# Performance work log

Hardware: AMD Instinct MI355X
Metric: run time of the kernel (lower is better)

Reference implementation:

```python
import jax, jax.numpy as jnp
import numpy as np

K_UPPER = 196608  # number of smallest-|grad| positions to mask per sample


def setup_inputs() -> dict:
    key = jax.random.key(0)
    k1, k2 = jax.random.split(key)
    x = jax.random.normal(k1, (64, 3, 512, 512), dtype=jnp.float32)
    grad = jax.random.normal(k2, (64, 3, 512, 512), dtype=jnp.float32)
    return {"x": x, "grad": grad}


def _mask_low_gradient(x, grad):
    # x, grad: [B, C, H, W]
    B, C, H, W = x.shape
    hw = H * W
    flat_g = grad.reshape(B, -1)                                  # [B, C*H*W]
    # _sort: k smallest absolute gradients -> top_k of negated abs (unsorted ok)
    _neg_vals, idx = jax.lax.top_k(-jnp.abs(flat_g), K_UPPER)     # idx: [B, K]
    # channel containing each selected flat index (matches the torch range test)
    ch = idx // hw                                                # [B, K]
    xc = x.reshape(B, C, hw)
    # Faithful to source: torch slice [start:channel_indexes] EXCLUDES the last
    # element of each channel when computing min/max.
    mn = jnp.min(xc[:, :, : hw - 1], axis=-1)                     # [B, C]
    mx = jnp.max(xc[:, :, : hw - 1], axis=-1)                     # [B, C]
    lo = jnp.take_along_axis(mn, ch, axis=1)                      # [B, K]
    hi = jnp.take_along_axis(mx, ch, axis=1)                      # [B, K]
    # uniform fill in [lo, hi) per masked element
    u = jax.random.uniform(jax.random.key(42), idx.shape, dtype=x.dtype)
    fill = lo + u * (hi - lo)                                     # [B, K]
    flat_x = x.reshape(B, -1)
    out = flat_x.at[jnp.arange(B)[:, None], idx].set(fill)
    return out.reshape(x.shape)


def reference(x, grad):
    return _mask_low_gradient(x, grad)
```

## Files before the change

### kernel.cpp

```cpp
#include <hip/hip_runtime.h>
#include <stdint.h>

#define TPB 256
#define TPS 1024

constexpr int BN   = 64;
constexpr int CCH  = 3;
constexpr int HWS  = 262144;
constexpr int LOG_HW = 18;
constexpr int NPS  = 786432;
constexpr int KSEL = 196608;
constexpr int KCAP = 200704;
constexpr int NB_T = 32;
constexpr int CH_T = NPS / NB_T;
constexpr int NB_S = 4;
constexpr int CH_S = KCAP / NB_S;
constexpr int TILE = 4096;
constexpr int NBINS = 2048;
constexpr int SUB  = 8;

constexpr int WS_MN   = 0;
constexpr int WS_MX   = 192;
constexpr int WS_V1   = 384;
constexpr int WS_B1   = 448;
constexpr int WS_GS   = 640;
constexpr int WS_KP   = 704;
constexpr int WS_CNT  = 768;
constexpr int WS_COFF = 2816;
constexpr int WS_MNP  = 4864;
constexpr int WS_MXP  = 6400;
constexpr int WS_THA  = 8192;
constexpr int WS_THB  = WS_THA + BN * NBINS;
constexpr int WS_H0   = WS_THB + BN * NBINS;
constexpr int WS_H1   = WS_H0 + BN * 256 * NB_S;
constexpr int WS_H2   = WS_H1 + BN * 256 * NB_S;
constexpr int WS_H3   = WS_H2 + BN * 256 * NB_S;
constexpr size_t WS_FIX_END = (size_t)WS_H3 + (size_t)BN * 256 * NB_S;
constexpr size_t RECW = (size_t)BN * KCAP * 2;
constexpr size_t WS_NEEDED_BYTES = (WS_FIX_END + 2 * RECW) * 4;

__device__ __forceinline__ unsigned rotl32(unsigned x, int r) { return (x << r) | (x >> (32 - r)); }

__device__ __forceinline__ void tf4(unsigned& x0, unsigned& x1, int a, int b, int c, int d) {
  x0 += x1; x1 = rotl32(x1, a); x1 ^= x0;
  x0 += x1; x1 = rotl32(x1, b); x1 ^= x0;
  x0 += x1; x1 = rotl32(x1, c); x1 ^= x0;
  x0 += x1; x1 = rotl32(x1, d); x1 ^= x0;
}

__device__ __forceinline__ void threefry2x32(unsigned k0, unsigned k1, unsigned c0, unsigned c1,
                                             unsigned& o0, unsigned& o1) {
  const unsigned ks2 = k0 ^ k1 ^ 0x1BD11BDAu;
  unsigned x0 = c0 + k0, x1 = c1 + k1;
  tf4(x0, x1, 13, 15, 26, 6);  x0 += k1;  x1 += ks2 + 1u;
  tf4(x0, x1, 17, 29, 16, 24); x0 += ks2; x1 += k0 + 2u;
  tf4(x0, x1, 13, 15, 26, 6);  x0 += k0;  x1 += k1 + 3u;
  tf4(x0, x1, 17, 29, 16, 24); x0 += k1;  x1 += ks2 + 4u;
  tf4(x0, x1, 13, 15, 26, 6);  x0 += ks2; x1 += k0 + 5u;
  o0 = x0; o1 = x1;
}

__global__ __launch_bounds__(TPB) void k_zero(unsigned* __restrict__ p, int n) {
  int i = blockIdx.x * TPB + threadIdx.x;
  if (i < n) p[i] = 0u;
}

__global__ __launch_bounds__(TPB) void k_copymn(const float4* __restrict__ x,
                                                float4* __restrict__ o,
                                                unsigned* __restrict__ ws) {
  __shared__ float smn[TPB], smx[TPB];
  const int g = blockIdx.x;
  const int bc = g / SUB, sub = g - bc * SUB;
  const int Q4 = HWS / 4 / SUB;
  const size_t base4 = (size_t)bc * (HWS / 4) + (size_t)sub * Q4;
  const bool last = (sub == SUB - 1);
  const int tid = threadIdx.x;
  float lo = 3.4e38f, hi = -3.4e38f;
  for (int i = tid; i < Q4; i += TPB) {
    float4 v = x[base4 + i];
    o[base4 + i] = v;
    if (last && i == Q4 - 1) {
      lo = fminf(lo, fminf(fminf(v.x, v.y), v.z));
      hi = fmaxf(hi, fmaxf(fmaxf(v.x, v.y), v.z));
    } else {
      lo = fminf(lo, fminf(fminf(v.x, v.y), fminf(v.z, v.w)));
      hi = fmaxf(hi, fmaxf(fmaxf(v.x, v.y), fmaxf(v.z, v.w)));
    }
  }
  smn[tid] = lo; smx[tid] = hi; __syncthreads();
  for (int s = TPB / 2; s > 0; s >>= 1) {
    if (tid < s) { smn[tid] = fminf(smn[tid], smn[tid + s]); smx[tid] = fmaxf(smx[tid], smx[tid + s]); }
    __syncthreads();
  }
  if (tid == 0) {
    ((float*)(ws + WS_MNP))[g] = smn[0];
    ((float*)(ws + WS_MXP))[g] = smx[0];
  }
}

__global__ __launch_bounds__(TPB) void k_mnfin(unsigned* __restrict__ ws) {
  const int t = threadIdx.x;
  if (t < BN * CCH) {
    const float* mnp = (const float*)(ws + WS_MNP);
    const float* mxp = (const float*)(ws + WS_MXP);
    float lo = 3.4e38f, hi = -3.4e38f;
    for (int s = 0; s < SUB; ++s) {
      lo = fminf(lo, mnp[t * SUB + s]);
      hi = fmaxf(hi, mxp[t * SUB + s]);
    }
    ((float*)(ws + WS_MN))[t] = lo;
    ((float*)(ws + WS_MX))[t] = hi;
  }
}

__global__ __launch_bounds__(TPB) void k_thrA(const unsigned* __restrict__ gb, unsigned* __restrict__ hist) {
  __shared__ unsigned h[NBINS];
  const int b = blockIdx.y, blk = blockIdx.x, tid = threadIdx.x;
  for (int v = tid; v < NBINS; v += TPB) h[v] = 0u;
  __syncthreads();
  const uint4* g4 = (const uint4*)(gb + (size_t)b * NPS + (size_t)blk * CH_T);
  for (int i = tid; i < CH_T / 4; i += TPB) {
    uint4 v = g4[i];
    atomicAdd(&h[(v.x & 0x7FFFFFFFu) >> 21], 1u);
    atomicAdd(&h[(v.y & 0x7FFFFFFFu) >> 21], 1u);
    atomicAdd(&h[(v.z & 0x7FFFFFFFu) >> 21], 1u);
    atomicAdd(&h[(v.w & 0x7FFFFFFFu) >> 21], 1u);
  }
  __syncthreads();
  unsigned* gh = hist + (size_t)b * NBINS;
  for (int v = tid; v < NBINS; v += TPB) if (h[v]) atomicAdd(&gh[v], h[v]);
}

__global__ __launch_bounds__(TPB) void k_thrB(const unsigned* __restrict__ gb,
                                              unsigned* __restrict__ hist,
                                              const unsigned* __restrict__ ws) {
  __shared__ unsigned h[NBINS];
  const int b = blockIdx.y, blk = blockIdx.x, tid = threadIdx.x;
  for (int v = tid; v < NBINS; v += TPB) h[v] = 0u;
  __syncthreads();
  const unsigned sel = ws[WS_V1 + b];
  const uint4* g4 = (const uint4*)(gb + (size_t)b * NPS + (size_t)blk * CH_T);
  for (int i = tid; i < CH_T / 4; i += TPB) {
    uint4 v = g4[i];
    unsigned a0 = v.x & 0x7FFFFFFFu, a1 = v.y & 0x7FFFFFFFu;
    unsigned a2 = v.z & 0x7FFFFFFFu, a3 = v.w & 0x7FFFFFFFu;
    if ((a0 >> 21) == sel) atomicAdd(&h[(a0 >> 10) & 2047u], 1u);
    if ((a1 >> 21) == sel) atomicAdd(&h[(a1 >> 10) & 2047u], 1u);
    if ((a2 >> 21) == sel) atomicAdd(&h[(a2 >> 10) & 2047u], 1u);
    if ((a3 >> 21) == sel) atomicAdd(&h[(a3 >> 10) & 2047u], 1u);
  }
  __syncthreads();
  unsigned* gh = hist + (size_t)b * NBINS;
  for (int v = tid; v < NBINS; v += TPB) if (h[v]) atomicAdd(&gh[v], h[v]);
}

__global__ __launch_bounds__(TPB) void k_find(const unsigned* __restrict__ hist,
                                              unsigned* __restrict__ ws, int mode) {
  __shared__ unsigned part[TPB];
  const int b = blockIdx.x, tid = threadIdx.x;
  const unsigned* h = hist + (size_t)b * NBINS;
  const int per = NBINS / TPB;
  const unsigned Kt = (mode == 0) ? (unsigned)KSEL : (unsigned)KSEL - ws[WS_B1 + b];
  unsigned vals[8];
  unsigned s = 0;
  for (int j = 0; j < per; ++j) { vals[j] = h[tid * per + j]; s += vals[j]; }
  part[tid] = s; __syncthreads();
  for (int off = 1; off < TPB; off <<= 1) {
    unsigned t = (tid >= off) ? part[tid - off] : 0u;
    __syncthreads(); part[tid] += t; __syncthreads();
  }
  unsigned run = part[tid] - s;
  for (int j = 0; j < per; ++j) {
    const unsigned lo = run, c = vals[j];
    run += c;
    if (lo < Kt && Kt <= run) {
      const unsigned v = (unsigned)(tid * per + j);
      if (mode == 0) {
        ws[WS_V1 + b] = v; ws[WS_B1 + b] = lo;
      } else {
        const unsigned T22 = (ws[WS_V1 + b] << 11) | v;
        ws[WS_GS + b] = (T22 << 10) | 1023u;
        unsigned kp = ws[WS_B1 + b] + lo + c;
        if (kp > (unsigned)KCAP) kp = (unsigned)KCAP;
        ws[WS_KP + b] = kp;
      }
    }
  }
}

__global__ __launch_bounds__(TPB) void k_ccount(const unsigned* __restrict__ gb, unsigned* __restrict__ ws) {
  __shared__ unsigned r[TPB];
  const int b = blockIdx.y, blk = blockIdx.x, tid = threadIdx.x;
  const unsigned G = ws[WS_GS + b];
  const uint4* g4 = (const uint4*)(gb + (size_t)b * NPS + (size_t)blk * CH_T);
  unsigned c = 0;
  for (int i = tid; i < CH_T / 4; i += TPB) {
    uint4 v = g4[i];
    c += (unsigned)((v.x & 0x7FFFFFFFu) <= G) + (unsigned)((v.y & 0x7FFFFFFFu) <= G)
       + (unsigned)((v.z & 0x7FFFFFFFu) <= G) + (unsigned)((v.w & 0x7FFFFFFFu) <= G);
  }
  r[tid] = c; __syncthreads();
  for (int s = TPB / 2; s > 0; s >>= 1) { if (tid < s) r[tid] += r[tid + s]; __syncthreads(); }
  if (tid == 0) ws[WS_CNT + b * NB_T + blk] = r[0];
}

__global__ void k_cscan(unsigned* __restrict__ ws) {
  const int b = blockIdx.x;
  if (threadIdx.x == 0) {
    unsigned run = 0;
    for (int j = 0; j < NB_T; ++j) {
      unsigned t = ws[WS_CNT + b * NB_T + j];
      ws[WS_COFF + b * NB_T + j] = run;
      run += t;
    }
  }
}

__global__ __launch_bounds__(TPB) void k_cscatter(const unsigned* __restrict__ gb,
                                                  const unsigned* __restrict__ ws,
                                                  uint2* __restrict__ outR,
                                                  unsigned* __restrict__ H0) {
  __shared__ unsigned h2[256 * NB_S];
  __shared__ unsigned waveTot[4];
  __shared__ unsigned runBase;
  const int b = blockIdx.y, blk = blockIdx.x, tid = threadIdx.x;
  const int lane = tid & 63, wv = tid >> 6;
  const unsigned long long ltm = (1ull << lane) - 1ull;
  const unsigned G = ws[WS_GS + b];
  for (int e = tid; e < 256 * NB_S; e += TPB) h2[e] = 0u;
  if (tid == 0) runBase = ws[WS_COFF + b * NB_T + blk];
  __syncthreads();
  const unsigned* g = gb + (size_t)b * NPS;
  uint2* oR = outR + (size_t)b * KCAP;
  const unsigned c0 = (unsigned)blk * CH_T;
  for (int t = 0; t < CH_T / 1024; ++t) {
    const unsigned base = c0 + (unsigned)t * 1024u + (unsigned)wv * 256u;
    unsigned key[4], wloc[4];
    bool sel[4];
    unsigned run = 0;
#pragma unroll
    for (int c = 0; c < 4; ++c) {
      const unsigned i = base + (unsigned)c * 64u + (unsigned)lane;
      key[c] = g[i] & 0x7FFFFFFFu;
      sel[c] = (key[c] <= G);
      unsigned long long m = __ballot(sel[c]);
      wloc[c] = run + (unsigned)__popcll(m & ltm);
      run += (unsigned)__popcll(m);
    }
    if (lane == 0) waveTot[wv] = run;
    __syncthreads();
    unsigned wpre = 0;
    for (int w = 0; w < wv; ++w) wpre += waveTot[w];
    const unsigned rb = runBase;
#pragma unroll
    for (int c = 0; c < 4; ++c) {
      if (sel[c]) {
        const unsigned pos = rb + wpre + wloc[c];
        if (pos < (unsigned)KCAP) {
          const unsigned i = base + (unsigned)c * 64u + (unsigned)lane;
          uint2 r; r.x = i; r.y = key[c];
          oR[pos] = r;
          atomicAdd(&h2[(key[c] & 255u) * NB_S + pos / (unsigned)CH_S], 1u);
        }
      }
    }
    __syncthreads();
    if (tid == 0) runBase += waveTot[0] + waveTot[1] + waveTot[2] + waveTot[3];
  }
  __syncthreads();
  unsigned* Hb = H0 + (size_t)b * 256 * NB_S;
  for (int e = tid; e < 256 * NB_S; e += TPB) {
    unsigned c = h2[e];
    if (c) atomicAdd(&Hb[e], c);
  }
}

__global__ __launch_bounds__(TPB) void k_hscan(unsigned* __restrict__ H) {
  __shared__ unsigned wsum[4];
  const int b = blockIdx.x, tid = threadIdx.x;
  const int lane = tid & 63, wv = tid >> 6;
  unsigned* Hb = H + (size_t)b * 256 * NB_S;
  unsigned row[NB_S];
  unsigned run = 0;
#pragma unroll
  for (int k = 0; k < NB_S; ++k) {
    unsigned t = Hb[tid * NB_S + k];
    row[k] = run; run += t;
  }
  unsigned incl = run;
  for (int off = 1; off < 64; off <<= 1) {
    unsigned t = __shfl_up(incl, off, 64);
    if (lane >= off) incl += t;
  }
  if (lane == 63) wsum[wv] = incl;
  __syncthreads();
  unsigned wpre = 0;
  for (int w = 0; w < wv; ++w) wpre += wsum[w];
  const unsigned excl = incl - run + wpre;
#pragma unroll
  for (int k = 0; k < NB_S; ++k) Hb[tid * NB_S + k] = row[k] + excl;
}

template<int FINAL>
__global__ __launch_bounds__(TPS) void k_sort8(const uint2* __restrict__ inR,
                                               uint2* __restrict__ outR,
                                               const unsigned* __restrict__ Hcur,
                                               unsigned* __restrict__ Hnext,
                                               const unsigned* __restrict__ ws,
                                               float* __restrict__ outF,
                                               int shift) {
  __shared__ unsigned wh[16][256];
  __shared__ unsigned gout[256];
  __shared__ unsigned gbase[256];
  __shared__ unsigned wsum[4];
  __shared__ uint2    stg[FINAL ? 1 : TILE];
  __shared__ unsigned h2[FINAL ? 1 : 256 * NB_S];
  const int b = blockIdx.y, blk = blockIdx.x, tid = threadIdx.x;
  const int lane = tid & 63, wv = tid >> 6;
  const unsigned long long ltm = (1ull << lane) - 1ull;
  const unsigned kp = min(ws[WS_KP + b], (unsigned)KCAP);
  const unsigned s0 = (unsigned)blk * CH_S;
  const unsigned s1 = min(s0 + (unsigned)CH_S, kp);
  const uint2* in = inR + (size_t)b * KCAP;
  uint2* out = outR + (size_t)b * KCAP;

  for (int d = tid; d < 256; d += TPS) gbase[d] = Hcur[((size_t)b * 256 + d) * NB_S + blk];
  if (!FINAL) for (int e = tid; e < 256 * NB_S; e += TPS) h2[e] = 0u;
  __syncthreads();

  for (unsigned t0 = s0; t0 < s1; t0 += (unsigned)TILE) {
    { uint4* w4 = (uint4*)&wh[0][0];
      w4[tid] = make_uint4(0u, 0u, 0u, 0u); }
    __syncthreads();

    unsigned key[4], idx[4], wloc[4], dig[4];
    bool val[4];
    const unsigned wbase = t0 + (unsigned)wv * 256u;
#pragma unroll
    for (int c = 0; c < 4; ++c) {
      const unsigned i = wbase + (unsigned)c * 64u + (unsigned)lane;
      val[c] = (i < s1);
      uint2 r = val[c] ? in[i] : make_uint2(0u, 0u);
      idx[c] = r.x; key[c] = r.y;
      dig[c] = (key[c] >> shift) & 255u;
      unsigned long long peers = __ballot(val[c]);
#pragma unroll
      for (int bit = 0; bit < 8; ++bit) {
        unsigned long long bb = __ballot(val[c] && ((dig[c] >> bit) & 1u));
        peers &= ((dig[c] >> bit) & 1u) ? bb : ~bb;
      }
      const unsigned before = (unsigned)__popcll(peers & ltm);
      int ldr = __ffsll((unsigned long long)peers) - 1;
      if (ldr < 0) ldr = 0;
      unsigned old = 0;
      if (val[c] && lane == ldr) old = atomicAdd(&wh[wv][dig[c]], (unsigned)__popcll(peers));
      old = __shfl(old, ldr, 64);
      wloc[c] = old + before;
    }
    __syncthreads();

    unsigned incl = 0, tot = 0;
    if (tid < 256) {
      const unsigned d = (unsigned)tid;
#pragma unroll
      for (int w = 0; w < 16; ++w) tot += wh[w][d];
      incl = tot;
      for (int off = 1; off < 64; off <<= 1) {
        unsigned t = __shfl_up(incl, off, 64);
        if (lane >= off) incl += t;
      }
      if (lane == 63) wsum[wv] = incl;
    }
    __syncthreads();
    if (tid < 256) {
      const unsigned d = (unsigned)tid;
      unsigned wpre = 0;
      for (int w = 0; w < wv; ++w) wpre += wsum[w];
      const unsigned tstart = incl - tot + wpre;
      const unsigned g = gbase[d];
      gout[d] = g - tstart;
      gbase[d] = g + tot;
      unsigned run = tstart;
#pragma unroll
      for (int w = 0; w < 16; ++w) { const unsigned t = wh[w][d]; wh[w][d] = run; run += t; }
    }
    __syncthreads();

    if (!FINAL) {
#pragma unroll
      for (int c = 0; c < 4; ++c) {
        if (val[c]) {
          uint2 r; r.x = idx[c]; r.y = key[c];
          stg[wh[wv][dig[c]] + wloc[c]] = r;
        }
      }
      __syncthreads();
      const unsigned nt = min((unsigned)TILE, s1 - t0);
      for (unsigned j = tid; j < nt; j += TPS) {
        const uint2 r = stg[j];
        const unsigned d = (r.y >> shift) & 255u;
        const unsigned pos = gout[d] + j;
        out[pos] = r;
        const unsigned nd = (r.y >> (shift + 8)) & 255u;
        atomicAdd(&h2[nd * NB_S + pos / (unsigned)CH_S], 1u);
      }
    } else {
#pragma unroll
      for (int c = 0; c < 4; ++c) {
        if (val[c]) {
          const unsigned rank = gout[dig[c]] + wh[wv][dig[c]] + wloc[c];
          if (rank < (unsigned)KSEL) {
            const unsigned p = (unsigned)b * (unsigned)KSEL + rank;
            unsigned o0, o1;
            threefry2x32(0u, 42u, 0u, p, o0, o1);
            const unsigned bits = o0 ^ o1;
            const float u = __uint_as_float((bits >> 9) | 0x3f800000u) - 1.0f;
            const unsigned ch = idx[c] >> LOG_HW;
            const float lo = ((const float*)(ws + WS_MN))[b * CCH + ch];
            const float hi = ((const float*)(ws + WS_MX))[b * CCH + ch];
            outF[(size_t)b * NPS + idx[c]] = lo + u * (hi - lo);
          }
        }
      }
    }
    __syncthreads();
  }

  if (!FINAL) {
    unsigned* Hb = Hnext + (size_t)b * 256 * NB_S;
    for (int e = tid; e < 256 * NB_S; e += TPS) {
      unsigned c = h2[e];
      if (c) atomicAdd(&Hb[e], c);
    }
  }
}

extern "C" void kernel_launch(void* const* d_in, const int* in_sizes, int n_in,
                              void* d_out, int out_size, void* d_ws, size_t ws_size,
                              hipStream_t stream) {
  const float* x = (const float*)d_in[0];
  const unsigned* gb = (const unsigned*)d_in[1];
  float* out = (float*)d_out;
  unsigned* ws = (unsigned*)d_ws;
  if (ws_size < WS_NEEDED_BYTES) return;

  uint2* bufA = (uint2*)(ws + WS_FIX_END);
  uint2* bufB = (uint2*)(ws + WS_FIX_END + RECW);
  unsigned* H0 = ws + WS_H0;
  unsigned* H1 = ws + WS_H1;
  unsigned* H2 = ws + WS_H2;
  unsigned* H3 = ws + WS_H3;

  dim3 blk(TPB);
  dim3 sblk(TPS);

  k_copymn<<<dim3(BN * CCH * SUB), blk, 0, stream>>>((const float4*)x, (float4*)out, ws);
  k_mnfin<<<dim3(1), blk, 0, stream>>>(ws);
  {
    const int nz = (int)(WS_FIX_END - WS_THA);
    k_zero<<<dim3((nz + TPB - 1) / TPB), blk, 0, stream>>>(ws + WS_THA, nz);
  }

  k_thrA<<<dim3(NB_T, BN), blk, 0, stream>>>(gb, ws + WS_THA);
  k_find<<<dim3(BN), blk, 0, stream>>>(ws + WS_THA, ws, 0);
  k_thrB<<<dim3(NB_T, BN), blk, 0, stream>>>(gb, ws + WS_THB, ws);
  k_find<<<dim3(BN), blk, 0, stream>>>(ws + WS_THB, ws, 1);

  k_ccount<<<dim3(NB_T, BN), blk, 0, stream>>>(gb, ws);
  k_cscan<<<dim3(BN), dim3(64), 0, stream>>>(ws);
  k_cscatter<<<dim3(NB_T, BN), blk, 0, stream>>>(gb, ws, bufA, H0);

  k_hscan<<<dim3(BN), blk, 0, stream>>>(H0);
  k_sort8<0><<<dim3(NB_S, BN), sblk, 0, stream>>>(bufA, bufB, H0, H1, ws, out, 0);
  k_hscan<<<dim3(BN), blk, 0, stream>>>(H1);
  k_sort8<0><<<dim3(NB_S, BN), sblk, 0, stream>>>(bufB, bufA, H1, H2, ws, out, 8);
  k_hscan<<<dim3(BN), blk, 0, stream>>>(H2);
  k_sort8<0><<<dim3(NB_S, BN), sblk, 0, stream>>>(bufA, bufB, H2, H3, ws, out, 16);
  k_hscan<<<dim3(BN), blk, 0, stream>>>(H3);
  k_sort8<1><<<dim3(NB_S, BN), sblk, 0, stream>>>(bufB, (uint2*)nullptr, H3, (unsigned*)nullptr, ws, out, 24);
}
```

Baseline: 817.4 us.

## Sort compacted-position keys, defer scatter to a fused copy-and-fill pass

The first sort pass now reads bare keys and uses each candidate's compacted position as the payload, so the compaction scatter writes 4 bytes per candidate instead of 8. The final sort pass no longer scatters random fills into the output. It writes each candidate's rank into a fill map indexed by compacted position. A new coalesced kernel then copies x to out, recomputes the compaction positions, and applies fills in place. This removes the separate copy pass and the random output scatter. The cost is re-reading grad and x in the fill pass. Compaction grid and sort block counts are also doubled (64 and 8 blocks) to add parallelism.

After: 798.2 us. 1.02x faster.

```diff
diff --git a/kernel.cpp b/kernel.cpp
--- a/kernel.cpp
+++ b/kernel.cpp
@@ -13,7 +13,9 @@
 constexpr int KCAP = 200704;
 constexpr int NB_T = 32;
 constexpr int CH_T = NPS / NB_T;
-constexpr int NB_S = 4;
+constexpr int NB_C = 64;
+constexpr int CH_C = NPS / NB_C;
+constexpr int NB_S = 8;
 constexpr int CH_S = KCAP / NB_S;
 constexpr int TILE = 4096;
 constexpr int NBINS = 2048;
@@ -23,13 +25,13 @@
 constexpr int WS_MX   = 192;
 constexpr int WS_V1   = 384;
 constexpr int WS_B1   = 448;
-constexpr int WS_GS   = 640;
-constexpr int WS_KP   = 704;
-constexpr int WS_CNT  = 768;
-constexpr int WS_COFF = 2816;
-constexpr int WS_MNP  = 4864;
-constexpr int WS_MXP  = 6400;
-constexpr int WS_THA  = 8192;
+constexpr int WS_GS   = 512;
+constexpr int WS_KP   = 576;
+constexpr int WS_CNT  = 640;
+constexpr int WS_COFF = WS_CNT + BN * NB_C;
+constexpr int WS_MNP  = WS_COFF + BN * NB_C;
+constexpr int WS_MXP  = WS_MNP + BN * CCH * SUB;
+constexpr int WS_THA  = WS_MXP + BN * CCH * SUB;
 constexpr int WS_THB  = WS_THA + BN * NBINS;
 constexpr int WS_H0   = WS_THB + BN * NBINS;
 constexpr int WS_H1   = WS_H0 + BN * 256 * NB_S;
@@ -65,9 +67,8 @@
   if (i < n) p[i] = 0u;
 }
 
-__global__ __launch_bounds__(TPB) void k_copymn(const float4* __restrict__ x,
-                                                float4* __restrict__ o,
-                                                unsigned* __restrict__ ws) {
+__global__ __launch_bounds__(TPB) void k_mnmx(const float4* __restrict__ x,
+                                              unsigned* __restrict__ ws) {
   __shared__ float smn[TPB], smx[TPB];
   const int g = blockIdx.x;
   const int bc = g / SUB, sub = g - bc * SUB;
@@ -78,7 +79,6 @@
   float lo = 3.4e38f, hi = -3.4e38f;
   for (int i = tid; i < Q4; i += TPB) {
     float4 v = x[base4 + i];
-    o[base4 + i] = v;
     if (last && i == Q4 - 1) {
       lo = fminf(lo, fminf(fminf(v.x, v.y), v.z));
       hi = fmaxf(hi, fmaxf(fmaxf(v.x, v.y), v.z));
@@ -192,25 +192,25 @@
   __shared__ unsigned r[TPB];
   const int b = blockIdx.y, blk = blockIdx.x, tid = threadIdx.x;
   const unsigned G = ws[WS_GS + b];
-  const uint4* g4 = (const uint4*)(gb + (size_t)b * NPS + (size_t)blk * CH_T);
+  const uint4* g4 = (const uint4*)(gb + (size_t)b * NPS + (size_t)blk * CH_C);
   unsigned c = 0;
-  for (int i = tid; i < CH_T / 4; i += TPB) {
+  for (int i = tid; i < CH_C / 4; i += TPB) {
     uint4 v = g4[i];
     c += (unsigned)((v.x & 0x7FFFFFFFu) <= G) + (unsigned)((v.y & 0x7FFFFFFFu) <= G)
        + (unsigned)((v.z & 0x7FFFFFFFu) <= G) + (unsigned)((v.w & 0x7FFFFFFFu) <= G);
   }
   r[tid] = c; __syncthreads();
   for (int s = TPB / 2; s > 0; s >>= 1) { if (tid < s) r[tid] += r[tid + s]; __syncthreads(); }
-  if (tid == 0) ws[WS_CNT + b * NB_T + blk] = r[0];
+  if (tid == 0) ws[WS_CNT + b * NB_C + blk] = r[0];
 }
 
 __global__ void k_cscan(unsigned* __restrict__ ws) {
   const int b = blockIdx.x;
   if (threadIdx.x == 0) {
     unsigned run = 0;
-    for (int j = 0; j < NB_T; ++j) {
-      unsigned t = ws[WS_CNT + b * NB_T + j];
-      ws[WS_COFF + b * NB_T + j] = run;
+    for (int j = 0; j < NB_C; ++j) {
+      unsigned t = ws[WS_CNT + b * NB_C + j];
+      ws[WS_COFF + b * NB_C + j] = run;
       run += t;
     }
   }
@@ -218,54 +218,51 @@
 
 __global__ __launch_bounds__(TPB) void k_cscatter(const unsigned* __restrict__ gb,
                                                   const unsigned* __restrict__ ws,
-                                                  uint2* __restrict__ outR,
+                                                  unsigned* __restrict__ keyArr,
                                                   unsigned* __restrict__ H0) {
   __shared__ unsigned h2[256 * NB_S];
   __shared__ unsigned waveTot[4];
   __shared__ unsigned runBase;
   const int b = blockIdx.y, blk = blockIdx.x, tid = threadIdx.x;
   const int lane = tid & 63, wv = tid >> 6;
-  const unsigned long long ltm = (1ull << lane) - 1ull;
   const unsigned G = ws[WS_GS + b];
   for (int e = tid; e < 256 * NB_S; e += TPB) h2[e] = 0u;
-  if (tid == 0) runBase = ws[WS_COFF + b * NB_T + blk];
-  __syncthreads();
-  const unsigned* g = gb + (size_t)b * NPS;
-  uint2* oR = outR + (size_t)b * KCAP;
-  const unsigned c0 = (unsigned)blk * CH_T;
-  for (int t = 0; t < CH_T / 1024; ++t) {
-    const unsigned base = c0 + (unsigned)t * 1024u + (unsigned)wv * 256u;
-    unsigned key[4], wloc[4];
-    bool sel[4];
-    unsigned run = 0;
+  if (tid == 0) runBase = ws[WS_COFF + b * NB_C + blk];
+  __syncthreads();
+  const uint4* g4 = (const uint4*)(gb + (size_t)b * NPS + (size_t)blk * CH_C);
+  unsigned* ka = keyArr + (size_t)b * KCAP;
+  for (int t = 0; t < CH_C / 1024; ++t) {
+    const uint4 v = g4[t * 256 + tid];
+    unsigned k[4] = { v.x & 0x7FFFFFFFu, v.y & 0x7FFFFFFFu, v.z & 0x7FFFFFFFu, v.w & 0x7FFFFFFFu };
+    bool s[4];
+    unsigned cnt = 0;
+#pragma unroll
+    for (int c = 0; c < 4; ++c) { s[c] = (k[c] <= G); cnt += (unsigned)s[c]; }
+    unsigned incl = cnt;
+    for (int off = 1; off < 64; off <<= 1) {
+      unsigned u = __shfl_up(incl, off, 64);
+      if (lane >= off) incl += u;
+    }
+    if (lane == 63) waveTot[wv] = incl;
+    __syncthreads();
+    const unsigned wt0 = waveTot[0], wt1 = waveTot[1], wt2 = waveTot[2], wt3 = waveTot[3];
+    unsigned wpre = 0;
+    if (wv > 0) wpre += wt0;
+    if (wv > 1) wpre += wt1;
+    if (wv > 2) wpre += wt2;
+    unsigned pos = runBase + wpre + (incl - cnt);
 #pragma unroll
     for (int c = 0; c < 4; ++c) {
-      const unsigned i = base + (unsigned)c * 64u + (unsigned)lane;
-      key[c] = g[i] & 0x7FFFFFFFu;
-      sel[c] = (key[c] <= G);
-      unsigned long long m = __ballot(sel[c]);
-      wloc[c] = run + (unsigned)__popcll(m & ltm);
-      run += (unsigned)__popcll(m);
-    }
-    if (lane == 0) waveTot[wv] = run;
-    __syncthreads();
-    unsigned wpre = 0;
-    for (int w = 0; w < wv; ++w) wpre += waveTot[w];
-    const unsigned rb = runBase;
-#pragma unroll
-    for (int c = 0; c < 4; ++c) {
-      if (sel[c]) {
-        const unsigned pos = rb + wpre + wloc[c];
+      if (s[c]) {
         if (pos < (unsigned)KCAP) {
-          const unsigned i = base + (unsigned)c * 64u + (unsigned)lane;
-          uint2 r; r.x = i; r.y = key[c];
-          oR[pos] = r;
-          atomicAdd(&h2[(key[c] & 255u) * NB_S + pos / (unsigned)CH_S], 1u);
+          ka[pos] = k[c];
+          atomicAdd(&h2[(k[c] & 255u) * NB_S + pos / (unsigned)CH_S], 1u);
         }
-      }
-    }
-    __syncthreads();
-    if (tid == 0) runBase += waveTot[0] + waveTot[1] + waveTot[2] + waveTot[3];
+        ++pos;
+      }
+    }
+    __syncthreads();
+    if (tid == 0) runBase += wt0 + wt1 + wt2 + wt3;
   }
   __syncthreads();
   unsigned* Hb = H0 + (size_t)b * 256 * NB_S;
@@ -301,31 +298,34 @@
   for (int k = 0; k < NB_S; ++k) Hb[tid * NB_S + k] = row[k] + excl;
 }
 
-template<int FINAL>
-__global__ __launch_bounds__(TPS) void k_sort8(const uint2* __restrict__ inR,
+template<int MODE>
+__global__ __launch_bounds__(TPS) void k_sort8(const unsigned* __restrict__ keyIn,
+                                               const uint2* __restrict__ inR,
                                                uint2* __restrict__ outR,
+                                               unsigned* __restrict__ fillmap,
                                                const unsigned* __restrict__ Hcur,
                                                unsigned* __restrict__ Hnext,
                                                const unsigned* __restrict__ ws,
-                                               float* __restrict__ outF,
                                                int shift) {
   __shared__ unsigned wh[16][256];
   __shared__ unsigned gout[256];
   __shared__ unsigned gbase[256];
   __shared__ unsigned wsum[4];
-  __shared__ uint2    stg[FINAL ? 1 : TILE];
-  __shared__ unsigned h2[FINAL ? 1 : 256 * NB_S];
+  __shared__ uint2    stg[(MODE == 2) ? 1 : TILE];
+  __shared__ unsigned h2[(MODE == 2) ? 1 : 256 * NB_S];
   const int b = blockIdx.y, blk = blockIdx.x, tid = threadIdx.x;
   const int lane = tid & 63, wv = tid >> 6;
   const unsigned long long ltm = (1ull << lane) - 1ull;
   const unsigned kp = min(ws[WS_KP + b], (unsigned)KCAP);
   const unsigned s0 = (unsigned)blk * CH_S;
   const unsigned s1 = min(s0 + (unsigned)CH_S, kp);
+  const unsigned* ki = keyIn + (size_t)b * KCAP;
   const uint2* in = inR + (size_t)b * KCAP;
   uint2* out = outR + (size_t)b * KCAP;
+  unsigned* fm = fillmap + (size_t)b * KCAP;
 
   for (int d = tid; d < 256; d += TPS) gbase[d] = Hcur[((size_t)b * 256 + d) * NB_S + blk];
-  if (!FINAL) for (int e = tid; e < 256 * NB_S; e += TPS) h2[e] = 0u;
+  if (MODE != 2) for (int e = tid; e < 256 * NB_S; e += TPS) h2[e] = 0u;
   __syncthreads();
 
   for (unsigned t0 = s0; t0 < s1; t0 += (unsigned)TILE) {
@@ -333,15 +333,15 @@
       w4[tid] = make_uint4(0u, 0u, 0u, 0u); }
     __syncthreads();
 
-    unsigned key[4], idx[4], wloc[4], dig[4];
+    unsigned key[4], cpp[4], wloc[4], dig[4];
     bool val[4];
     const unsigned wbase = t0 + (unsigned)wv * 256u;
 #pragma unroll
     for (int c = 0; c < 4; ++c) {
       const unsigned i = wbase + (unsigned)c * 64u + (unsigned)lane;
       val[c] = (i < s1);
-      uint2 r = val[c] ? in[i] : make_uint2(0u, 0u);
-      idx[c] = r.x; key[c] = r.y;
+      if (MODE == 0) { cpp[c] = i; key[c] = val[c] ? ki[i] : 0u; }
+      else { uint2 r = val[c] ? in[i] : make_uint2(0u, 0u); cpp[c] = r.x; key[c] = r.y; }
       dig[c] = (key[c] >> shift) & 255u;
       unsigned long long peers = __ballot(val[c]);
 #pragma unroll
@@ -386,11 +386,11 @@
     }
     __syncthreads();
 
-    if (!FINAL) {
+    if (MODE != 2) {
 #pragma unroll
       for (int c = 0; c < 4; ++c) {
         if (val[c]) {
-          uint2 r; r.x = idx[c]; r.y = key[c];
+          uint2 r; r.x = cpp[c]; r.y = key[c];
           stg[wh[wv][dig[c]] + wloc[c]] = r;
         }
       }
@@ -409,29 +409,88 @@
       for (int c = 0; c < 4; ++c) {
         if (val[c]) {
           const unsigned rank = gout[dig[c]] + wh[wv][dig[c]] + wloc[c];
-          if (rank < (unsigned)KSEL) {
-            const unsigned p = (unsigned)b * (unsigned)KSEL + rank;
+          fm[cpp[c]] = (rank < (unsigned)KSEL) ? rank : 0xFFFFFFFFu;
+        }
+      }
+    }
+    __syncthreads();
+  }
+
+  if (MODE != 2) {
+    unsigned* Hb = Hnext + (size_t)b * 256 * NB_S;
+    for (int e = tid; e < 256 * NB_S; e += TPS) {
+      unsigned c = h2[e];
+      if (c) atomicAdd(&Hb[e], c);
+    }
+  }
+}
+
+__global__ __launch_bounds__(TPB) void k_fill(const uint4* __restrict__ x4,
+                                              const unsigned* __restrict__ gb,
+                                              const unsigned* __restrict__ fillmap,
+                                              const unsigned* __restrict__ ws,
+                                              float4* __restrict__ out4) {
+  __shared__ unsigned waveTot[4];
+  __shared__ unsigned runBase;
+  const int b = blockIdx.y, blk = blockIdx.x, tid = threadIdx.x;
+  const int lane = tid & 63, wv = tid >> 6;
+  const unsigned G = ws[WS_GS + b];
+  const unsigned kp = min(ws[WS_KP + b], (unsigned)KCAP);
+  if (tid == 0) runBase = ws[WS_COFF + b * NB_C + blk];
+  __syncthreads();
+  const size_t base4 = ((size_t)b * NPS + (size_t)blk * CH_C) / 4;
+  const uint4* g4 = (const uint4*)(gb + (size_t)b * NPS + (size_t)blk * CH_C);
+  const unsigned* fm = fillmap + (size_t)b * KCAP;
+  const float* mnf = (const float*)(ws + WS_MN);
+  const float* mxf = (const float*)(ws + WS_MX);
+  const unsigned ebase = (unsigned)blk * (unsigned)CH_C;
+
+  for (int t = 0; t < CH_C / 1024; ++t) {
+    const uint4 gv = g4[t * 256 + tid];
+    uint4 xv = ((const uint4*)x4)[base4 + t * 256 + tid];
+    unsigned k[4] = { gv.x & 0x7FFFFFFFu, gv.y & 0x7FFFFFFFu, gv.z & 0x7FFFFFFFu, gv.w & 0x7FFFFFFFu };
+    bool s[4];
+    unsigned cnt = 0;
+#pragma unroll
+    for (int c = 0; c < 4; ++c) { s[c] = (k[c] <= G); cnt += (unsigned)s[c]; }
+    unsigned incl = cnt;
+    for (int off = 1; off < 64; off <<= 1) {
+      unsigned u = __shfl_up(incl, off, 64);
+      if (lane >= off) incl += u;
+    }
+    if (lane == 63) waveTot[wv] = incl;
+    __syncthreads();
+    const unsigned wt0 = waveTot[0], wt1 = waveTot[1], wt2 = waveTot[2], wt3 = waveTot[3];
+    unsigned wpre = 0;
+    if (wv > 0) wpre += wt0;
+    if (wv > 1) wpre += wt1;
+    if (wv > 2) wpre += wt2;
+    unsigned pos = runBase + wpre + (incl - cnt);
+    unsigned* xw = (unsigned*)&xv;
+#pragma unroll
+    for (int c = 0; c < 4; ++c) {
+      if (s[c]) {
+        if (pos < kp) {
+          const unsigned r = fm[pos];
+          if (r != 0xFFFFFFFFu) {
+            const unsigned p = (unsigned)b * (unsigned)KSEL + r;
             unsigned o0, o1;
             threefry2x32(0u, 42u, 0u, p, o0, o1);
             const unsigned bits = o0 ^ o1;
             const float u = __uint_as_float((bits >> 9) | 0x3f800000u) - 1.0f;
-            const unsigned ch = idx[c] >> LOG_HW;
-            const float lo = ((const float*)(ws + WS_MN))[b * CCH + ch];
-            const float hi = ((const float*)(ws + WS_MX))[b * CCH + ch];
-            outF[(size_t)b * NPS + idx[c]] = lo + u * (hi - lo);
+            const unsigned e = ebase + (unsigned)t * 1024u + (unsigned)tid * 4u + (unsigned)c;
+            const unsigned ch = e >> LOG_HW;
+            const float lo = mnf[b * CCH + ch];
+            const float hi = mxf[b * CCH + ch];
+            xw[c] = __float_as_uint(lo + u * (hi - lo));
           }
         }
-      }
-    }
-    __syncthreads();
-  }
-
-  if (!FINAL) {
-    unsigned* Hb = Hnext + (size_t)b * 256 * NB_S;
-    for (int e = tid; e < 256 * NB_S; e += TPS) {
-      unsigned c = h2[e];
-      if (c) atomicAdd(&Hb[e], c);
-    }
+        ++pos;
+      }
+    }
+    ((uint4*)out4)[base4 + t * 256 + tid] = xv;
+    __syncthreads();
+    if (tid == 0) runBase += wt0 + wt1 + wt2 + wt3;
   }
 }
 
@@ -444,8 +503,8 @@
   unsigned* ws = (unsigned*)d_ws;
   if (ws_size < WS_NEEDED_BYTES) return;
 
-  uint2* bufA = (uint2*)(ws + WS_FIX_END);
-  uint2* bufB = (uint2*)(ws + WS_FIX_END + RECW);
+  unsigned* R1 = ws + WS_FIX_END;
+  unsigned* R2 = ws + WS_FIX_END + RECW;
   unsigned* H0 = ws + WS_H0;
   unsigned* H1 = ws + WS_H1;
   unsigned* H2 = ws + WS_H2;
@@ -454,7 +513,7 @@
   dim3 blk(TPB);
   dim3 sblk(TPS);
 
-  k_copymn<<<dim3(BN * CCH * SUB), blk, 0, stream>>>((const float4*)x, (float4*)out, ws);
+  k_mnmx<<<dim3(BN * CCH * SUB), blk, 0, stream>>>((const float4*)x, ws);
   k_mnfin<<<dim3(1), blk, 0, stream>>>(ws);
   {
     const int nz = (int)(WS_FIX_END - WS_THA);
@@ -466,16 +525,18 @@
   k_thrB<<<dim3(NB_T, BN), blk, 0, stream>>>(gb, ws + WS_THB, ws);
   k_find<<<dim3(BN), blk, 0, stream>>>(ws + WS_THB, ws, 1);
 
-  k_ccount<<<dim3(NB_T, BN), blk, 0, stream>>>(gb, ws);
+  k_ccount<<<dim3(NB_C, BN), blk, 0, stream>>>(gb, ws);
   k_cscan<<<dim3(BN), dim3(64), 0, stream>>>(ws);
-  k_cscatter<<<dim3(NB_T, BN), blk, 0, stream>>>(gb, ws, bufA, H0);
+  k_cscatter<<<dim3(NB_C, BN), blk, 0, stream>>>(gb, ws, R1, H0);
 
   k_hscan<<<dim3(BN), blk, 0, stream>>>(H0);
-  k_sort8<0><<<dim3(NB_S, BN), sblk, 0, stream>>>(bufA, bufB, H0, H1, ws, out, 0);
+  k_sort8<0><<<dim3(NB_S, BN), sblk, 0, stream>>>(R1, (const uint2*)nullptr, (uint2*)R2, nullptr, H0, H1, ws, 0);
   k_hscan<<<dim3(BN), blk, 0, stream>>>(H1);
-  k_sort8<0><<<dim3(NB_S, BN), sblk, 0, stream>>>(bufB, bufA, H1, H2, ws, out, 8);
+  k_sort8<1><<<dim3(NB_S, BN), sblk, 0, stream>>>(nullptr, (const uint2*)R2, (uint2*)R1, nullptr, H1, H2, ws, 8);
   k_hscan<<<dim3(BN), blk, 0, stream>>>(H2);
-  k_sort8<0><<<dim3(NB_S, BN), sblk, 0, stream>>>(bufA, bufB, H2, H3, ws, out, 16);
+  k_sort8<1><<<dim3(NB_S, BN), sblk, 0, stream>>>(nullptr, (const uint2*)R1, (uint2*)R2, nullptr, H2, H3, ws, 16);
   k_hscan<<<dim3(BN), blk, 0, stream>>>(H3);
-  k_sort8<1><<<dim3(NB_S, BN), sblk, 0, stream>>>(bufB, (uint2*)nullptr, H3, (unsigned*)nullptr, ws, out, 24);
-}
+  k_sort8<2><<<dim3(NB_S, BN), sblk, 0, stream>>>(nullptr, (const uint2*)R2, (uint2*)nullptr, R1, H3, nullptr, ws, 24);
+
+  k_fill<<<dim3(NB_C, BN), blk, 0, stream>>>((const uint4*)x, gb, R1, ws, (float4*)out);
+}
```
